# Performance work log

Hardware: AMD Instinct MI355X
Metric: run time of the kernel (lower is better)

The kernel has to match this reference:

```python
import jax, jax.numpy as jnp
import numpy as np

N = 100000   # atoms
E = 1000000  # edges per conv (includes N self loops)
R = 10000    # residues
P = 50000    # correspondence pairs
C = 25       # in_channels
D_IN = 7 + C # local_nn input width
RADII = (5.0, 8.5, 10.0)
EPS = 1e-12


def _init_lin(key, fi, fo):
    kw, kb = jax.random.split(key)
    s = 1.0 / np.sqrt(fi)
    W = jax.random.uniform(kw, (fi, fo), minval=-s, maxval=s, dtype=jnp.float32)
    b = jax.random.uniform(kb, (fo,), minval=-s, maxval=s, dtype=jnp.float32)
    return W, b


def setup_inputs() -> dict:
    key = jax.random.key(0)
    ks = jax.random.split(key, 24)
    x = jax.random.normal(ks[0], (N, C), dtype=jnp.float32)
    pos = jax.random.normal(ks[1], (N, 3), dtype=jnp.float32) * 10.0
    nrm = jax.random.normal(ks[2], (N, 3), dtype=jnp.float32)
    nrm = nrm / jnp.linalg.norm(nrm, axis=1, keepdims=True)

    def make_edges(k):
        rnd = jax.random.randint(k, (2, E - N), 0, N, dtype=jnp.int32)
        loops = jnp.tile(jnp.arange(N, dtype=jnp.int32)[None, :], (2, 1))
        return jnp.concatenate([rnd, loops], axis=1)  # [2, E], self loops appended

    ei2, ei3, ei4 = make_edges(ks[3]), make_edges(ks[4]), make_edges(ks[5])
    atom2res = (jnp.arange(N) * R // N).astype(jnp.int32)  # contiguous atom->residue blocks
    src_idx = jax.random.randint(ks[6], (P,), 0, R, dtype=jnp.int32)
    tgt_idx = jax.random.randint(ks[7], (P,), 0, R, dtype=jnp.int32)

    inp = {"x": x, "pos": pos, "normal": nrm, "ei2": ei2, "ei3": ei3, "ei4": ei4,
           "atom2res": atom2res, "src_idx": src_idx, "tgt_idx": tgt_idx}
    for i, n in enumerate(["c2", "c3", "c4"]):
        W1, b1 = _init_lin(ks[8 + 2 * i], D_IN, D_IN)
        W2, b2 = _init_lin(ks[9 + 2 * i], D_IN, 128)
        inp[n + "_W1"], inp[n + "_b1"] = W1, b1
        inp[n + "_W2"], inp[n + "_b2"] = W2, b2
    inp["Wa"], inp["ba"] = _init_lin(ks[14], 384, 256)
    inp["Wr"], inp["br"] = _init_lin(ks[15], 256, 512)
    inp["Wl"], inp["bl"] = _init_lin(ks[16], 512, 1)
    return inp


def _angle(a, b):
    # torch_geometric get_angle: atan2(||cross||, dot); eps keeps grad finite at 0
    cr = jnp.cross(a, b)
    return jnp.arctan2(jnp.sqrt(jnp.sum(cr * cr, axis=1) + EPS), jnp.sum(a * b, axis=1))


def _ppf_conv(x, pos, normal, ei, radius, W1, b1, W2, b2):
    j, i = ei[0], ei[1]  # source, target
    d = pos[j] - pos[i]                                   # [E,3]
    dist = jnp.sqrt(jnp.sum(d * d, axis=1) + EPS)
    a1 = _angle(normal[i], d)
    a2 = _angle(normal[j], d)
    a3 = _angle(normal[i], normal[j])
    ppf = jnp.stack([dist / radius,
                     jnp.sin(a1), jnp.cos(a1),
                     jnp.sin(a2), jnp.cos(a2),
                     jnp.sin(a3), jnp.cos(a3)], axis=1)   # [E,7]
    msg = jnp.concatenate([x[j], ppf], axis=1)            # [E, 7+C]
    h = jnp.tanh(msg @ W1 + b1)                           # local_nn layer 1 (Dropout: eval)
    h = jnp.tanh(h @ W2 + b2)                             # local_nn layer 2 -> [E,128]
    return jax.ops.segment_max(h, i, num_segments=pos.shape[0])  # max aggr


def reference(x, pos, normal, ei2, ei3, ei4, atom2res, src_idx, tgt_idx,
              c2_W1, c2_b1, c2_W2, c2_b2,
              c3_W1, c3_b1, c3_W2, c3_b2,
              c4_W1, c4_b1, c4_W2, c4_b2,
              Wa, ba, Wr, br, Wl, bl):
    o2 = _ppf_conv(x, pos, normal, ei2, RADII[0], c2_W1, c2_b1, c2_W2, c2_b2)
    o3 = _ppf_conv(x, pos, normal, ei3, RADII[1], c3_W1, c3_b1, c3_W2, c3_b2)
    o4 = _ppf_conv(x, pos, normal, ei4, RADII[2], c4_W1, c4_b1, c4_W2, c4_b2)
    atom = jnp.tanh(jnp.concatenate([o2, o3, o4], axis=1) @ Wa + ba)   # [N,256]
    res = jax.ops.segment_max(atom, atom2res, num_segments=R)          # global_max_pool
    res = jnp.tanh(res @ Wr + br)                                      # [R,512]
    out = (res[src_idx] - res[tgt_idx]) @ Wl + bl                      # [P,1] logits
    return out
```

## Files before the change

### kernel.cpp

```cpp
#include <hip/hip_runtime.h>
#include <hip/hip_bf16.h>

#define NN 100000
#define EE 1000000
#define RR 10000
#define PP 50000

typedef _Float16 f16x8 __attribute__((ext_vector_type(8)));
typedef _Float16 f16x2 __attribute__((ext_vector_type(2)));
typedef float f32x4 __attribute__((ext_vector_type(4)));
typedef unsigned long long ull;

__device__ __forceinline__ float tfast(float x){
    float e = __expf(2.0f * x);
    return 1.0f - __fdividef(2.0f, e + 1.0f);
}
__device__ __forceinline__ unsigned encf(float f){
    unsigned u = __float_as_uint(f);
    return (u & 0x80000000u) ? ~u : (u | 0x80000000u);
}
__device__ __forceinline__ float decf(unsigned u){
    return (u & 0x80000000u) ? __uint_as_float(u ^ 0x80000000u) : __uint_as_float(~u);
}
__device__ __forceinline__ unsigned pk2(float a, float b){
    _Float16 ha = (_Float16)a, hb = (_Float16)b;
    unsigned short ua = __builtin_bit_cast(unsigned short, ha);
    unsigned short ub = __builtin_bit_cast(unsigned short, hb);
    return (unsigned)ua | ((unsigned)ub << 16);
}
__device__ __forceinline__ ull pk4(float a, float b, float c, float d){
    return ((ull)pk2(c, d) << 32) | (ull)pk2(a, b);
}

__global__ __launch_bounds__(256) void k_xw1(
    const float* __restrict__ x,
    const float* __restrict__ W1_0, const float* __restrict__ b1_0,
    const float* __restrict__ W1_1, const float* __restrict__ b1_1,
    const float* __restrict__ W1_2, const float* __restrict__ b1_2,
    _Float16* __restrict__ xw1)
{
    int g = blockIdx.x * 256 + threadIdx.x;
    if (g >= 3 * NN * 8) return;
    int cv  = g / (NN * 8);
    int rem = g - cv * (NN * 8);
    int n   = rem >> 3, cg = rem & 7;
    const float* W1 = (cv == 0) ? W1_0 : ((cv == 1) ? W1_1 : W1_2);
    const float* b1 = (cv == 0) ? b1_0 : ((cv == 1) ? b1_1 : b1_2);
    float4 acc = *(const float4*)&b1[cg * 4];
    const float* xr = x + (size_t)n * 25;
    #pragma unroll
    for (int m = 0; m < 25; m++){
        float xv = xr[m];
        float4 w = *(const float4*)&W1[m * 32 + cg * 4];
        acc.x = fmaf(xv, w.x, acc.x); acc.y = fmaf(xv, w.y, acc.y);
        acc.z = fmaf(xv, w.z, acc.z); acc.w = fmaf(xv, w.w, acc.w);
    }
    *(ull*)&xw1[((size_t)cv * NN + n) * 32 + cg * 4] = pk4(acc.x, acc.y, acc.z, acc.w);
}

__global__ __launch_bounds__(256) void k_prep(const float* __restrict__ Wa, _Float16* __restrict__ BF)
{
    int g = blockIdx.x * 256 + threadIdx.x;
    int o = g * 4;
    int j0 = o & 7;
    int t1 = o >> 3;
    int ln = t1 & 15;
    int t2 = t1 >> 4;
    int kg = t2 & 3;
    int t3 = t2 >> 2;
    int c  = t3 % 12;
    int nt = t3 / 12;
    int colg = nt * 16 + ln;
    int krow = c * 32 + kg * 8 + j0;
    float w0 = Wa[(size_t)(krow + 0) * 256 + colg];
    float w1 = Wa[(size_t)(krow + 1) * 256 + colg];
    float w2 = Wa[(size_t)(krow + 2) * 256 + colg];
    float w3 = Wa[(size_t)(krow + 3) * 256 + colg];
    *(ull*)&BF[o] = pk4(w0, w1, w2, w3);
}

__global__ __launch_bounds__(256) void k_prepw(
    const float* __restrict__ W2_0, const float* __restrict__ W2_1, const float* __restrict__ W2_2,
    _Float16* __restrict__ W2F)
{
    int g = blockIdx.x * 256 + threadIdx.x;
    int cv = g >> 9;
    int f  = g & 511;
    int ln = f & 15;
    int kg = (f >> 4) & 3;
    int mt = f >> 6;
    const float* W2 = (cv == 0) ? W2_0 : ((cv == 1) ? W2_1 : W2_2);
    f16x8 v;
    #pragma unroll
    for (int jj = 0; jj < 8; jj++)
        v[jj] = (_Float16)W2[(kg * 8 + jj) * 128 + mt * 16 + ln];
    ((f16x8*)W2F)[g] = v;
}

__global__ __launch_bounds__(256) void k_hist(
    const int* __restrict__ e2, const int* __restrict__ e3, const int* __restrict__ e4,
    unsigned* __restrict__ cur)
{
    long g = (long)blockIdx.x * 256 + threadIdx.x;
    if (g >= 3L * EE) return;
    int cv = (int)(g / EE);
    int e  = (int)(g - (long)cv * EE);
    const int* ei = (cv == 0) ? e2 : ((cv == 1) ? e3 : e4);
    int tg = ei[EE + e];
    atomicAdd(&cur[cv * NN + tg], 1u);
}

__global__ __launch_bounds__(1024) void k_scan(unsigned* __restrict__ cur)
{
    int cv = blockIdx.x;
    unsigned* a = cur + (size_t)cv * NN;
    __shared__ unsigned wsum[16];
    __shared__ unsigned carry;
    if (threadIdx.x == 0) carry = 0;
    int lane = threadIdx.x & 63, wv = threadIdx.x >> 6;
    for (int base = 0; base < NN; base += 1024){
        int idx = base + threadIdx.x;
        unsigned v = (idx < NN) ? a[idx] : 0u;
        unsigned s = v;
        #pragma unroll
        for (int d = 1; d < 64; d <<= 1){
            unsigned t = (unsigned)__shfl_up((int)s, d);
            if (lane >= d) s += t;
        }
        if (lane == 63) wsum[wv] = s;
        __syncthreads();
        if (wv == 0 && lane < 16){
            unsigned t = wsum[lane];
            #pragma unroll
            for (int d = 1; d < 16; d <<= 1){
                unsigned u = (unsigned)__shfl_up((int)t, d);
                if (lane >= d) t += u;
            }
            wsum[lane] = t;
        }
        __syncthreads();
        unsigned waveoff = (wv == 0) ? 0u : wsum[wv - 1];
        unsigned excl = carry + waveoff + s - v;
        if (idx < NN) a[idx] = excl;
        __syncthreads();
        if (threadIdx.x == 0) carry += wsum[15];
        __syncthreads();
    }
}

__global__ __launch_bounds__(256) void k_scatter(
    const int* __restrict__ e2, const int* __restrict__ e3, const int* __restrict__ e4,
    unsigned* __restrict__ cur, ull* __restrict__ esort)
{
    long g = (long)blockIdx.x * 256 + threadIdx.x;
    if (g >= 3L * EE) return;
    int cv = (int)(g / EE);
    int e  = (int)(g - (long)cv * EE);
    const int* ei = (cv == 0) ? e2 : ((cv == 1) ? e3 : e4);
    int j  = ei[e];
    int tg = ei[EE + e];
    unsigned p = atomicAdd(&cur[cv * NN + tg], 1u);
    esort[(size_t)cv * EE + p] = ((ull)(unsigned)tg << 32) | (unsigned)j;
}

__global__ __launch_bounds__(256) void k_conv(
    const ull* __restrict__ esort,
    const _Float16* __restrict__ xw1,
    const float* __restrict__ pos, const float* __restrict__ nrm,
    const float* __restrict__ W1_0, const float* __restrict__ W1_1, const float* __restrict__ W1_2,
    const _Float16* __restrict__ W2F,
    const float* __restrict__ b2_0, const float* __restrict__ b2_1, const float* __restrict__ b2_2,
    unsigned* __restrict__ feat)
{
    const int cv = blockIdx.y;
    const float invR = (cv == 0) ? 0.2f : ((cv == 1) ? (1.0f / 8.5f) : 0.1f);
    const float* W1 = (cv == 0) ? W1_0 : ((cv == 1) ? W1_1 : W1_2);
    const float* b2 = (cv == 0) ? b2_0 : ((cv == 1) ? b2_1 : b2_2);
    const ull* eS = esort + (size_t)cv * EE;
    const _Float16* xw = xw1 + (size_t)cv * NN * 32;

    __shared__ __align__(16) _Float16 hS[128 * 32];
    __shared__ __align__(16) _Float16 sLds[128 * 128];
    __shared__ float w1p[224];
    __shared__ int tgtL[128];

    int tid = threadIdx.x;
    if (tid < 224) w1p[tid] = W1[800 + tid];

    int gbase = blockIdx.x * 128;
    int e     = tid & 127;
    int hlf   = tid >> 7;
    int eg = gbase + e; if (eg >= EE) eg = EE - 1;
    ull ev = eS[eg];
    int j  = (int)(unsigned)(ev & 0xffffffffu);
    int it = (int)(unsigned)(ev >> 32);
    if (hlf == 0) tgtL[e] = it;
    __syncthreads();

    float pix = pos[(size_t)it * 3 + 0], piy = pos[(size_t)it * 3 + 1], piz = pos[(size_t)it * 3 + 2];
    float pjx = pos[(size_t)j  * 3 + 0], pjy = pos[(size_t)j  * 3 + 1], pjz = pos[(size_t)j  * 3 + 2];
    float nix = nrm[(size_t)it * 3 + 0], niy = nrm[(size_t)it * 3 + 1], niz = nrm[(size_t)it * 3 + 2];
    float njx = nrm[(size_t)j  * 3 + 0], njy = nrm[(size_t)j  * 3 + 1], njz = nrm[(size_t)j  * 3 + 2];

    float dx = pjx - pix, dy = pjy - piy, dz = pjz - piz;
    float dist = sqrtf(dx * dx + dy * dy + dz * dz + 1e-12f);

    float cx = niy * dz - niz * dy, cyv = niz * dx - nix * dz, cz = nix * dy - niy * dx;
    float y1 = sqrtf(cx * cx + cyv * cyv + cz * cz + 1e-12f);
    float x1 = nix * dx + niy * dy + niz * dz;
    float ir = __frsqrt_rn(x1 * x1 + y1 * y1);
    float s1 = y1 * ir, c1 = x1 * ir;
    cx = njy * dz - njz * dy; cyv = njz * dx - njx * dz; cz = njx * dy - njy * dx;
    float y2 = sqrtf(cx * cx + cyv * cyv + cz * cz + 1e-12f);
    float x2 = njx * dx + njy * dy + njz * dz;
    ir = __frsqrt_rn(x2 * x2 + y2 * y2);
    float s2 = y2 * ir, c2 = x2 * ir;
    cx = niy * njz - niz * njy; cyv = niz * njx - nix * njz; cz = nix * njy - niy * njx;
    float y3 = sqrtf(cx * cx + cyv * cyv + cz * cz + 1e-12f);
    float x3 = nix * njx + niy * njy + niz * njz;
    ir = __frsqrt_rn(x3 * x3 + y3 * y3);
    float s3 = y3 * ir, c3 = x3 * ir;

    float ppf[7] = { dist * invR, s1, c1, s2, c2, s3, c3 };

    int ch0 = hlf * 16;
    float h16[16];
    {
        const f16x8* xr = (const f16x8*)(xw + (size_t)j * 32 + ch0);
        f16x8 v0 = xr[0], v1 = xr[1];
        #pragma unroll
        for (int q = 0; q < 8; q++){ h16[q] = (float)v0[q]; h16[8 + q] = (float)v1[q]; }
    }
    #pragma unroll
    for (int f = 0; f < 7; f++){
        float pv = ppf[f];
        const float4* w4 = (const float4*)&w1p[f * 32 + ch0];
        #pragma unroll
        for (int q = 0; q < 4; q++){
            float4 w = w4[q];
            h16[q*4+0] = fmaf(pv, w.x, h16[q*4+0]);
            h16[q*4+1] = fmaf(pv, w.y, h16[q*4+1]);
            h16[q*4+2] = fmaf(pv, w.z, h16[q*4+2]);
            h16[q*4+3] = fmaf(pv, w.w, h16[q*4+3]);
        }
    }
    #pragma unroll
    for (int c = 0; c < 16; c++) h16[c] = tfast(h16[c]);

    {
        f16x8 c0v, c1v;
        #pragma unroll
        for (int q = 0; q < 8; q++){ c0v[q] = (_Float16)h16[q]; c1v[q] = (_Float16)h16[8 + q]; }
        int key = (e >> 1) & 3;
        int kg0 = 2 * hlf;
        *(f16x8*)&hS[e * 32 + ((kg0     ) ^ key) * 8] = c0v;
        *(f16x8*)&hS[e * 32 + ((kg0 + 1) ^ key) * 8] = c1v;
    }
    __syncthreads();

    int lane = tid & 63, wv = tid >> 6;
    int ln15 = lane & 15, kg = lane >> 4;
    const f16x8* w2f = (const f16x8*)W2F + (size_t)cv * 512;
    f16x8 a[8];
    #pragma unroll
    for (int mt = 0; mt < 8; mt++)
        a[mt] = w2f[(mt * 4 + kg) * 16 + ln15];

    f32x4 acc[2][8];
    #pragma unroll
    for (int n = 0; n < 2; n++)
        #pragma unroll
        for (int mt = 0; mt < 8; mt++)
            acc[n][mt] = (f32x4){0.f, 0.f, 0.f, 0.f};

    #pragma unroll
    for (int nti = 0; nti < 2; nti++){
        int ee = (2 * wv + nti) * 16 + ln15;
        f16x8 b = *(const f16x8*)&hS[ee * 32 + (kg ^ ((ee >> 1) & 3)) * 8];
        #pragma unroll
        for (int mt = 0; mt < 8; mt++)
            acc[nti][mt] = __builtin_amdgcn_mfma_f32_16x16x32_f16(a[mt], b, acc[nti][mt], 0, 0, 0);
    }
    #pragma unroll
    for (int nti = 0; nti < 2; nti++){
        int ee  = (2 * wv + nti) * 16 + ln15;
        int key = ee & 15;
        #pragma unroll
        for (int parity = 0; parity < 2; parity++){
            #pragma unroll
            for (int q = 0; q < 4; q++){
                unsigned lo = pk2(acc[nti][parity + 0][q], acc[nti][parity + 2][q]);
                unsigned hi = pk2(acc[nti][parity + 4][q], acc[nti][parity + 6][q]);
                int u2 = parity * 16 + kg * 4 + q;
                ull v = ((ull)hi << 32) | lo;
                *(ull*)&sLds[ee * 128 + ((u2 ^ key) << 2)] = v;
            }
        }
    }
    __syncthreads();

    int egp = tid >> 5;
    int u   = tid & 31;
    float b2v0 = b2[u], b2v1 = b2[u + 32], b2v2 = b2[u + 64], b2v3 = b2[u + 96];
    int curT = -1;
    f16x2 m01 = (f16x2)(_Float16)(-60000.0f), m23 = m01;
    int ebase = egp * 16;
    #pragma unroll
    for (int er = 0; er < 16; er++){
        int ee = ebase + er;
        int tg = tgtL[ee];
        ull sv = *(const ull*)&sLds[ee * 128 + ((u ^ er) << 2)];
        f16x2 s01 = __builtin_bit_cast(f16x2, (unsigned)(sv & 0xffffffffu));
        f16x2 s23 = __builtin_bit_cast(f16x2, (unsigned)(sv >> 32));
        if (tg != curT){
            if (curT >= 0){
                unsigned* fp = &feat[(size_t)curT * 384 + cv * 128 + u];
                atomicMax(fp +  0, encf((float)m01[0] + b2v0));
                atomicMax(fp + 32, encf((float)m01[1] + b2v1));
                atomicMax(fp + 64, encf((float)m23[0] + b2v2));
                atomicMax(fp + 96, encf((float)m23[1] + b2v3));
            }
            curT = tg; m01 = s01; m23 = s23;
        } else {
            m01 = __builtin_elementwise_max(m01, s01);
            m23 = __builtin_elementwise_max(m23, s23);
        }
    }
    {
        unsigned* fp = &feat[(size_t)curT * 384 + cv * 128 + u];
        atomicMax(fp +  0, encf((float)m01[0] + b2v0));
        atomicMax(fp + 32, encf((float)m01[1] + b2v1));
        atomicMax(fp + 64, encf((float)m23[0] + b2v2));
        atomicMax(fp + 96, encf((float)m23[1] + b2v3));
    }
}

__global__ __launch_bounds__(256) void k_atom(
    const unsigned* __restrict__ feat, const _Float16* __restrict__ BF,
    const float* __restrict__ ba, float* __restrict__ resm)
{
    __shared__ __align__(16) char ldsbuf[81920];
    _Float16* Ah = (_Float16*)ldsbuf;
    float*    Cs = (float*)ldsbuf;

    int tid = threadIdx.x;
    size_t base = (size_t)blockIdx.x * 80 * 384;

    #pragma unroll
    for (int itr = 0; itr < 30; itr++){
        int idx = itr * 1024 + tid * 4;
        uint4 v = *(const uint4*)&feat[base + idx];
        int r = idx / 384;
        int k = idx - r * 384;
        float f0 = tfast(decf(v.x));
        float f1 = tfast(decf(v.y));
        float f2 = tfast(decf(v.z));
        float f3 = tfast(decf(v.w));
        int u = (k >> 3) ^ (r & 7);
        *(ull*)&Ah[r * 384 + u * 8 + (k & 7)] = pk4(f0, f1, f2, f3);
    }
    __syncthreads();

    int lane = tid & 63, wv = tid >> 6;
    int ln15 = lane & 15, kg = lane >> 4;
    f32x4 acc[5][4];
    #pragma unroll
    for (int mt = 0; mt < 5; mt++)
        #pragma unroll
        for (int nti = 0; nti < 4; nti++)
            acc[mt][nti] = (f32x4){0.f, 0.f, 0.f, 0.f};

    const f16x8* bfp = (const f16x8*)BF;
    #pragma unroll
    for (int c = 0; c < 12; c++){
        f16x8 af[5];
        #pragma unroll
        for (int mt = 0; mt < 5; mt++){
            int row = mt * 16 + ln15;
            af[mt] = *(const f16x8*)&Ah[row * 384 + (((c * 4 + kg) ^ (row & 7)) << 3)];
        }
        #pragma unroll
        for (int nti = 0; nti < 4; nti++){
            f16x8 b = bfp[(((wv * 4 + nti) * 12 + c) * 4 + kg) * 16 + ln15];
            #pragma unroll
            for (int mt = 0; mt < 5; mt++)
                acc[mt][nti] = __builtin_amdgcn_mfma_f32_16x16x32_f16(af[mt], b, acc[mt][nti], 0, 0, 0);
        }
    }
    __syncthreads();

    #pragma unroll
    for (int nti = 0; nti < 4; nti++){
        int col = wv * 64 + nti * 16 + ln15;
        float bac = ba[col];
        #pragma unroll
        for (int mt = 0; mt < 5; mt++){
            #pragma unroll
            for (int q = 0; q < 4; q++){
                int row = mt * 16 + kg * 4 + q;
                Cs[row * 256 + (col ^ (kg << 2))] = acc[mt][nti][q] + bac;
            }
        }
    }
    __syncthreads();

    int res0 = blockIdx.x * 8;
    #pragma unroll
    for (int o = 0; o < 8; o++){
        int out = o * 256 + tid;
        int r = out >> 8, cc = out & 255;
        float m = -3.0e38f;
        #pragma unroll
        for (int q = 0; q < 10; q++){
            int row = r * 10 + q;
            m = fmaxf(m, Cs[row * 256 + (cc ^ (((row >> 2) & 3) << 2))]);
        }
        resm[(size_t)(res0 + r) * 256 + cc] = tfast(m);
    }
}

__global__ __launch_bounds__(256) void k_res(
    const float* __restrict__ resm, const float* __restrict__ Wr,
    const float* __restrict__ br, const float* __restrict__ Wl,
    float* __restrict__ lw)
{
    __shared__ __align__(16) float As[16 * 16];
    __shared__ __align__(16) float Ws[16 * 512];
    __shared__ float lwL[16];
    int tid  = threadIdx.x;
    int row0 = blockIdx.x * 16;
    int colg = tid & 127, rowg = tid >> 7;
    int c0 = colg * 4;
    int lane = tid & 63;
    if (tid < 16) lwL[tid] = 0.0f;
    float4 acc[8];
    float4 brv = *(const float4*)&br[c0];
    #pragma unroll
    for (int r = 0; r < 8; r++) acc[r] = brv;

    for (int k0 = 0; k0 < 256; k0 += 16){
        __syncthreads();
        { int r = tid >> 4, k = tid & 15;
          As[tid] = resm[(size_t)(row0 + r) * 256 + k0 + k]; }
        #pragma unroll
        for (int t0 = 0; t0 < 32; t0++){
            int t = tid + t0 * 256;
            int k = t >> 9, c = t & 511;
            Ws[t] = Wr[(size_t)(k0 + k) * 512 + c];
        }
        __syncthreads();
        #pragma unroll
        for (int kk = 0; kk < 16; kk += 4){
            float4 w0 = *(const float4*)&Ws[(kk + 0) * 512 + c0];
            float4 w1 = *(const float4*)&Ws[(kk + 1) * 512 + c0];
            float4 w2 = *(const float4*)&Ws[(kk + 2) * 512 + c0];
            float4 w3 = *(const float4*)&Ws[(kk + 3) * 512 + c0];
            #pragma unroll
            for (int r = 0; r < 8; r++){
                const float4 a = *(const float4*)&As[(rowg * 8 + r) * 16 + kk];
                acc[r].x = fmaf(a.x, w0.x, fmaf(a.y, w1.x, fmaf(a.z, w2.x, fmaf(a.w, w3.x, acc[r].x))));
                acc[r].y = fmaf(a.x, w0.y, fmaf(a.y, w1.y, fmaf(a.z, w2.y, fmaf(a.w, w3.y, acc[r].y))));
                acc[r].z = fmaf(a.x, w0.z, fmaf(a.y, w1.z, fmaf(a.z, w2.z, fmaf(a.w, w3.z, acc[r].z))));
                acc[r].w = fmaf(a.x, w0.w, fmaf(a.y, w1.w, fmaf(a.z, w2.w, fmaf(a.w, w3.w, acc[r].w))));
            }
        }
    }
    float4 wl = *(const float4*)&Wl[c0];
    #pragma unroll
    for (int r = 0; r < 8; r++){
        float4 v = acc[r];
        float p = tfast(v.x) * wl.x + tfast(v.y) * wl.y + tfast(v.z) * wl.z + tfast(v.w) * wl.w;
        #pragma unroll
        for (int m = 1; m < 64; m <<= 1) p += __shfl_xor(p, m);
        if (lane == 0) atomicAdd(&lwL[rowg * 8 + r], p);
    }
    __syncthreads();
    if (tid < 16) lw[row0 + tid] = lwL[tid];
}

__global__ __launch_bounds__(256) void k_out(
    const float* __restrict__ lw, const int* __restrict__ src, const int* __restrict__ tgt,
    const float* __restrict__ bl, float* __restrict__ out)
{
    int p = blockIdx.x * 256 + threadIdx.x;
    if (p < PP) out[p] = lw[src[p]] - lw[tgt[p]] + bl[0];
}

extern "C" void kernel_launch(void* const* d_in, const int* in_sizes, int n_in,
                              void* d_out, int out_size, void* d_ws, size_t ws_size,
                              hipStream_t stream)
{
    const float* x    = (const float*)d_in[0];
    const float* pos  = (const float*)d_in[1];
    const float* nrm  = (const float*)d_in[2];
    const int*   ei2  = (const int*)d_in[3];
    const int*   ei3  = (const int*)d_in[4];
    const int*   ei4  = (const int*)d_in[5];
    const int*   srci = (const int*)d_in[7];
    const int*   tgti = (const int*)d_in[8];
    const float* c2W1 = (const float*)d_in[9];
    const float* c2b1 = (const float*)d_in[10];
    const float* c2W2 = (const float*)d_in[11];
    const float* c2b2 = (const float*)d_in[12];
    const float* c3W1 = (const float*)d_in[13];
    const float* c3b1 = (const float*)d_in[14];
    const float* c3W2 = (const float*)d_in[15];
    const float* c3b2 = (const float*)d_in[16];
    const float* c4W1 = (const float*)d_in[17];
    const float* c4b1 = (const float*)d_in[18];
    const float* c4W2 = (const float*)d_in[19];
    const float* c4b2 = (const float*)d_in[20];
    const float* Wa   = (const float*)d_in[21];
    const float* ba   = (const float*)d_in[22];
    const float* Wr   = (const float*)d_in[23];
    const float* br   = (const float*)d_in[24];
    const float* Wl   = (const float*)d_in[25];
    const float* bl   = (const float*)d_in[26];

    char* ws = (char*)d_ws;
    _Float16* xw1  = (_Float16*)(ws);
    _Float16* W2F  = (_Float16*)(ws +  19200000);
    _Float16* BF   = (_Float16*)(ws +  19224576);
    unsigned* cur  = (unsigned*)(ws +  19421184);
    ull*      esort= (ull*)     (ws +  20621312);
    unsigned* feat = (unsigned*)(ws +  44621312);
    float*    resm = (float*)   (ws + 198221312);
    float*    lw   = (float*)   (ws + 208461312);

    hipMemsetAsync(cur,  0, (size_t)3 * NN * 4, stream);
    hipMemsetAsync(feat, 0, (size_t)NN * 384 * 4, stream);

    k_xw1<<<9375, 256, 0, stream>>>(x, c2W1, c2b1, c3W1, c3b1, c4W1, c4b1, xw1);
    k_prep<<<96, 256, 0, stream>>>(Wa, BF);
    k_prepw<<<6, 256, 0, stream>>>(c2W2, c3W2, c4W2, W2F);
    k_hist<<<(3 * EE + 255) / 256, 256, 0, stream>>>(ei2, ei3, ei4, cur);
    k_scan<<<3, 1024, 0, stream>>>(cur);
    k_scatter<<<(3 * EE + 255) / 256, 256, 0, stream>>>(ei2, ei3, ei4, cur, esort);
    dim3 gconv((EE + 127) / 128, 3);
    k_conv<<<gconv, 256, 0, stream>>>(esort, xw1, pos, nrm,
                                      c2W1, c3W1, c4W1, W2F,
                                      c2b2, c3b2, c4b2, feat);
    k_atom<<<NN / 80, 256, 0, stream>>>(feat, BF, ba, resm);
    k_res<<<RR / 16, 256, 0, stream>>>(resm, Wr, br, Wl, lw);
    k_out<<<(PP + 255) / 256, 256, 0, stream>>>(lw, srci, tgti, bl, (float*)d_out);
}
```

Baseline: 950.9 us.

## Fuse preprocessing kernels, parallelize CSR scan, vectorize histogram and scatter

```diff
diff --git a/kernel.cpp b/kernel.cpp
--- a/kernel.cpp
+++ b/kernel.cpp
@@ -32,135 +32,171 @@
     return ((ull)pk2(c, d) << 32) | (ull)pk2(a, b);
 }
 
-__global__ __launch_bounds__(256) void k_xw1(
+__global__ __launch_bounds__(256) void k_pre(
     const float* __restrict__ x,
     const float* __restrict__ W1_0, const float* __restrict__ b1_0,
     const float* __restrict__ W1_1, const float* __restrict__ b1_1,
     const float* __restrict__ W1_2, const float* __restrict__ b1_2,
-    _Float16* __restrict__ xw1)
-{
-    int g = blockIdx.x * 256 + threadIdx.x;
-    if (g >= 3 * NN * 8) return;
-    int cv  = g / (NN * 8);
-    int rem = g - cv * (NN * 8);
-    int n   = rem >> 3, cg = rem & 7;
-    const float* W1 = (cv == 0) ? W1_0 : ((cv == 1) ? W1_1 : W1_2);
-    const float* b1 = (cv == 0) ? b1_0 : ((cv == 1) ? b1_1 : b1_2);
-    float4 acc = *(const float4*)&b1[cg * 4];
-    const float* xr = x + (size_t)n * 25;
-    #pragma unroll
-    for (int m = 0; m < 25; m++){
-        float xv = xr[m];
-        float4 w = *(const float4*)&W1[m * 32 + cg * 4];
-        acc.x = fmaf(xv, w.x, acc.x); acc.y = fmaf(xv, w.y, acc.y);
-        acc.z = fmaf(xv, w.z, acc.z); acc.w = fmaf(xv, w.w, acc.w);
-    }
-    *(ull*)&xw1[((size_t)cv * NN + n) * 32 + cg * 4] = pk4(acc.x, acc.y, acc.z, acc.w);
-}
-
-__global__ __launch_bounds__(256) void k_prep(const float* __restrict__ Wa, _Float16* __restrict__ BF)
-{
-    int g = blockIdx.x * 256 + threadIdx.x;
-    int o = g * 4;
-    int j0 = o & 7;
-    int t1 = o >> 3;
-    int ln = t1 & 15;
-    int t2 = t1 >> 4;
-    int kg = t2 & 3;
-    int t3 = t2 >> 2;
-    int c  = t3 % 12;
-    int nt = t3 / 12;
-    int colg = nt * 16 + ln;
-    int krow = c * 32 + kg * 8 + j0;
-    float w0 = Wa[(size_t)(krow + 0) * 256 + colg];
-    float w1 = Wa[(size_t)(krow + 1) * 256 + colg];
-    float w2 = Wa[(size_t)(krow + 2) * 256 + colg];
-    float w3 = Wa[(size_t)(krow + 3) * 256 + colg];
-    *(ull*)&BF[o] = pk4(w0, w1, w2, w3);
-}
-
-__global__ __launch_bounds__(256) void k_prepw(
+    _Float16* __restrict__ xw1,
+    const float* __restrict__ Wa, _Float16* __restrict__ BF,
     const float* __restrict__ W2_0, const float* __restrict__ W2_1, const float* __restrict__ W2_2,
-    _Float16* __restrict__ W2F)
-{
-    int g = blockIdx.x * 256 + threadIdx.x;
-    int cv = g >> 9;
-    int f  = g & 511;
-    int ln = f & 15;
-    int kg = (f >> 4) & 3;
-    int mt = f >> 6;
-    const float* W2 = (cv == 0) ? W2_0 : ((cv == 1) ? W2_1 : W2_2);
-    f16x8 v;
-    #pragma unroll
-    for (int jj = 0; jj < 8; jj++)
-        v[jj] = (_Float16)W2[(kg * 8 + jj) * 128 + mt * 16 + ln];
-    ((f16x8*)W2F)[g] = v;
-}
-
-__global__ __launch_bounds__(256) void k_hist(
+    _Float16* __restrict__ W2F,
     const int* __restrict__ e2, const int* __restrict__ e3, const int* __restrict__ e4,
-    unsigned* __restrict__ cur)
-{
-    long g = (long)blockIdx.x * 256 + threadIdx.x;
-    if (g >= 3L * EE) return;
-    int cv = (int)(g / EE);
-    int e  = (int)(g - (long)cv * EE);
-    const int* ei = (cv == 0) ? e2 : ((cv == 1) ? e3 : e4);
-    int tg = ei[EE + e];
-    atomicAdd(&cur[cv * NN + tg], 1u);
-}
-
-__global__ __launch_bounds__(1024) void k_scan(unsigned* __restrict__ cur)
-{
-    int cv = blockIdx.x;
+    unsigned* __restrict__ cur,
+    uint4* __restrict__ featz)
+{
+    int b = blockIdx.x, tid = threadIdx.x;
+    if (b < 9375){
+        int g = b * 256 + tid;
+        int cv  = g / (NN * 8);
+        int rem = g - cv * (NN * 8);
+        int n   = rem >> 3, cg = rem & 7;
+        const float* W1 = (cv == 0) ? W1_0 : ((cv == 1) ? W1_1 : W1_2);
+        const float* b1 = (cv == 0) ? b1_0 : ((cv == 1) ? b1_1 : b1_2);
+        float4 acc = *(const float4*)&b1[cg * 4];
+        const float* xr = x + (size_t)n * 25;
+        #pragma unroll
+        for (int m = 0; m < 25; m++){
+            float xv = xr[m];
+            float4 w = *(const float4*)&W1[m * 32 + cg * 4];
+            acc.x = fmaf(xv, w.x, acc.x); acc.y = fmaf(xv, w.y, acc.y);
+            acc.z = fmaf(xv, w.z, acc.z); acc.w = fmaf(xv, w.w, acc.w);
+        }
+        *(ull*)&xw1[((size_t)cv * NN + n) * 32 + cg * 4] = pk4(acc.x, acc.y, acc.z, acc.w);
+    } else if (b < 9471){
+        int g = (b - 9375) * 256 + tid;
+        int o = g * 4;
+        int j0 = o & 7;
+        int t1 = o >> 3;
+        int ln = t1 & 15;
+        int t2 = t1 >> 4;
+        int kg = t2 & 3;
+        int t3 = t2 >> 2;
+        int c  = t3 % 12;
+        int nt = t3 / 12;
+        int colg = nt * 16 + ln;
+        int krow = c * 32 + kg * 8 + j0;
+        float w0 = Wa[(size_t)(krow + 0) * 256 + colg];
+        float w1 = Wa[(size_t)(krow + 1) * 256 + colg];
+        float w2 = Wa[(size_t)(krow + 2) * 256 + colg];
+        float w3 = Wa[(size_t)(krow + 3) * 256 + colg];
+        *(ull*)&BF[o] = pk4(w0, w1, w2, w3);
+    } else if (b < 9477){
+        int g = (b - 9471) * 256 + tid;
+        int cv = g >> 9;
+        int f  = g & 511;
+        int ln = f & 15;
+        int kg = (f >> 4) & 3;
+        int mt = f >> 6;
+        const float* W2 = (cv == 0) ? W2_0 : ((cv == 1) ? W2_1 : W2_2);
+        f16x8 v;
+        #pragma unroll
+        for (int jj = 0; jj < 8; jj++)
+            v[jj] = (_Float16)W2[(kg * 8 + jj) * 128 + mt * 16 + ln];
+        ((f16x8*)W2F)[g] = v;
+    } else if (b < 12407){
+        int t4 = (b - 9477) * 256 + tid;
+        if (t4 < 750000){
+            long ge = (long)t4 * 4;
+            int cv = (int)(ge / EE);
+            int e  = (int)(ge - (long)cv * EE);
+            const int* ei = (cv == 0) ? e2 : ((cv == 1) ? e3 : e4);
+            uint4 ts = *(const uint4*)&ei[EE + e];
+            unsigned* cc = cur + (size_t)cv * NN;
+            atomicAdd(&cc[ts.x], 1u);
+            atomicAdd(&cc[ts.y], 1u);
+            atomicAdd(&cc[ts.z], 1u);
+            atomicAdd(&cc[ts.w], 1u);
+        }
+    } else {
+        size_t base = (size_t)(b - 12407) * 1024;
+        uint4 z = make_uint4(0u, 0u, 0u, 0u);
+        #pragma unroll
+        for (int k = 0; k < 4; k++)
+            featz[base + k * 256 + tid] = z;
+    }
+}
+
+__global__ __launch_bounds__(1024) void k_scanA(unsigned* __restrict__ cur, unsigned* __restrict__ totals)
+{
+    int c = blockIdx.x;
+    int cv = c / 98, lc = c - cv * 98;
     unsigned* a = cur + (size_t)cv * NN;
     __shared__ unsigned wsum[16];
-    __shared__ unsigned carry;
-    if (threadIdx.x == 0) carry = 0;
-    int lane = threadIdx.x & 63, wv = threadIdx.x >> 6;
-    for (int base = 0; base < NN; base += 1024){
-        int idx = base + threadIdx.x;
-        unsigned v = (idx < NN) ? a[idx] : 0u;
-        unsigned s = v;
-        #pragma unroll
-        for (int d = 1; d < 64; d <<= 1){
-            unsigned t = (unsigned)__shfl_up((int)s, d);
-            if (lane >= d) s += t;
-        }
-        if (lane == 63) wsum[wv] = s;
+    int tid = threadIdx.x, lane = tid & 63, wv = tid >> 6;
+    int idx = lc * 1024 + tid;
+    unsigned v = (idx < NN) ? a[idx] : 0u;
+    unsigned s = v;
+    #pragma unroll
+    for (int d = 1; d < 64; d <<= 1){
+        unsigned t = (unsigned)__shfl_up((int)s, d);
+        if (lane >= d) s += t;
+    }
+    if (lane == 63) wsum[wv] = s;
+    __syncthreads();
+    if (wv == 0 && lane < 16){
+        unsigned t = wsum[lane];
+        #pragma unroll
+        for (int d = 1; d < 16; d <<= 1){
+            unsigned u = (unsigned)__shfl_up((int)t, d);
+            if (lane >= d) t += u;
+        }
+        wsum[lane] = t;
+    }
+    __syncthreads();
+    unsigned waveoff = (wv == 0) ? 0u : wsum[wv - 1];
+    if (idx < NN) a[idx] = waveoff + s - v;
+    if (tid == 0) totals[c] = wsum[15];
+}
+
+__global__ __launch_bounds__(512) void k_scanB(unsigned* __restrict__ totals)
+{
+    __shared__ unsigned buf[294];
+    int tid = threadIdx.x;
+    unsigned own = 0;
+    if (tid < 294){ own = totals[tid]; buf[tid] = own; }
+    __syncthreads();
+    for (int d = 1; d < 98; d <<= 1){
+        unsigned add = 0;
+        if (tid < 294 && (tid % 98) >= d) add = buf[tid - d];
         __syncthreads();
-        if (wv == 0 && lane < 16){
-            unsigned t = wsum[lane];
-            #pragma unroll
-            for (int d = 1; d < 16; d <<= 1){
-                unsigned u = (unsigned)__shfl_up((int)t, d);
-                if (lane >= d) t += u;
-            }
-            wsum[lane] = t;
-        }
+        if (tid < 294) buf[tid] += add;
         __syncthreads();
-        unsigned waveoff = (wv == 0) ? 0u : wsum[wv - 1];
-        unsigned excl = carry + waveoff + s - v;
-        if (idx < NN) a[idx] = excl;
-        __syncthreads();
-        if (threadIdx.x == 0) carry += wsum[15];
-        __syncthreads();
-    }
+    }
+    if (tid < 294) totals[tid] = buf[tid] - own;
 }
 
 __global__ __launch_bounds__(256) void k_scatter(
     const int* __restrict__ e2, const int* __restrict__ e3, const int* __restrict__ e4,
-    unsigned* __restrict__ cur, ull* __restrict__ esort)
-{
-    long g = (long)blockIdx.x * 256 + threadIdx.x;
-    if (g >= 3L * EE) return;
-    int cv = (int)(g / EE);
-    int e  = (int)(g - (long)cv * EE);
+    unsigned* __restrict__ cur, const unsigned* __restrict__ totals, ull* __restrict__ esort)
+{
+    int t4 = blockIdx.x * 256 + threadIdx.x;
+    if (t4 >= 750000) return;
+    long ge = (long)t4 * 4;
+    int cv = (int)(ge / EE);
+    int e  = (int)(ge - (long)cv * EE);
     const int* ei = (cv == 0) ? e2 : ((cv == 1) ? e3 : e4);
-    int j  = ei[e];
-    int tg = ei[EE + e];
-    unsigned p = atomicAdd(&cur[cv * NN + tg], 1u);
-    esort[(size_t)cv * EE + p] = ((ull)(unsigned)tg << 32) | (unsigned)j;
+    uint4 js = *(const uint4*)&ei[e];
+    uint4 ts = *(const uint4*)&ei[EE + e];
+    unsigned* cc = cur + (size_t)cv * NN;
+    const unsigned* tc = totals + cv * 98;
+    ull* es = esort + (size_t)cv * EE;
+    {
+        unsigned p = atomicAdd(&cc[ts.x], 1u) + tc[ts.x >> 10];
+        es[p] = ((ull)ts.x << 32) | js.x;
+    }
+    {
+        unsigned p = atomicAdd(&cc[ts.y], 1u) + tc[ts.y >> 10];
+        es[p] = ((ull)ts.y << 32) | js.y;
+    }
+    {
+        unsigned p = atomicAdd(&cc[ts.z], 1u) + tc[ts.z >> 10];
+        es[p] = ((ull)ts.z << 32) | js.z;
+    }
+    {
+        unsigned p = atomicAdd(&cc[ts.w], 1u) + tc[ts.w >> 10];
+        es[p] = ((ull)ts.w << 32) | js.w;
+    }
 }
 
 __global__ __launch_bounds__(256) void k_conv(
@@ -518,24 +554,24 @@
     const float* bl   = (const float*)d_in[26];
 
     char* ws = (char*)d_ws;
-    _Float16* xw1  = (_Float16*)(ws);
-    _Float16* W2F  = (_Float16*)(ws +  19200000);
-    _Float16* BF   = (_Float16*)(ws +  19224576);
-    unsigned* cur  = (unsigned*)(ws +  19421184);
-    ull*      esort= (ull*)     (ws +  20621312);
-    unsigned* feat = (unsigned*)(ws +  44621312);
-    float*    resm = (float*)   (ws + 198221312);
-    float*    lw   = (float*)   (ws + 208461312);
-
-    hipMemsetAsync(cur,  0, (size_t)3 * NN * 4, stream);
-    hipMemsetAsync(feat, 0, (size_t)NN * 384 * 4, stream);
-
-    k_xw1<<<9375, 256, 0, stream>>>(x, c2W1, c2b1, c3W1, c3b1, c4W1, c4b1, xw1);
-    k_prep<<<96, 256, 0, stream>>>(Wa, BF);
-    k_prepw<<<6, 256, 0, stream>>>(c2W2, c3W2, c4W2, W2F);
-    k_hist<<<(3 * EE + 255) / 256, 256, 0, stream>>>(ei2, ei3, ei4, cur);
-    k_scan<<<3, 1024, 0, stream>>>(cur);
-    k_scatter<<<(3 * EE + 255) / 256, 256, 0, stream>>>(ei2, ei3, ei4, cur, esort);
+    _Float16* xw1   = (_Float16*)(ws);
+    _Float16* W2F   = (_Float16*)(ws +  19200000);
+    _Float16* BF    = (_Float16*)(ws +  19224576);
+    unsigned* cur   = (unsigned*)(ws +  19421184);
+    ull*      esort = (ull*)     (ws +  20621312);
+    unsigned* feat  = (unsigned*)(ws +  44621312);
+    float*    resm  = (float*)   (ws + 198221312);
+    float*    lw    = (float*)   (ws + 208461312);
+    unsigned* totals= (unsigned*)(ws + 208501312);
+
+    hipMemsetAsync(cur, 0, (size_t)3 * NN * 4, stream);
+
+    k_pre<<<21782, 256, 0, stream>>>(x, c2W1, c2b1, c3W1, c3b1, c4W1, c4b1, xw1,
+                                     Wa, BF, c2W2, c3W2, c4W2, W2F,
+                                     ei2, ei3, ei4, cur, (uint4*)feat);
+    k_scanA<<<294, 1024, 0, stream>>>(cur, totals);
+    k_scanB<<<1, 512, 0, stream>>>(totals);
+    k_scatter<<<2930, 256, 0, stream>>>(ei2, ei3, ei4, cur, totals, esort);
     dim3 gconv((EE + 127) / 128, 3);
     k_conv<<<gconv, 256, 0, stream>>>(esort, xw1, pos, nrm,
                                       c2W1, c3W1, c4W1, W2F,
```

New measurement: 873.0 us. -8.2%, faster.
